# Kernel optimization log

Measured on AMD Instinct MI355X. Metric: run time of the kernel, lower is better.

Reference implementation:

```python
import jax, jax.numpy as jnp
import numpy as np

DIM = 2048
N_HEADS = 16
N_KV_HEADS = 4
HEAD_DIM = DIM // N_HEADS  # 128
T = 2048


def setup_inputs() -> dict:
    key = jax.random.key(0)
    k1, k2, k3 = jax.random.split(key, 3)
    scale = 1.0 / np.sqrt(DIM)
    x = jax.random.normal(k1, (T, DIM), dtype=jnp.float32)
    # GQA-consistent fused QKV projection: q (n_h*hd) + k (n_kv*hd) + v (n_kv*hd)
    qkv_out = (N_HEADS + 2 * N_KV_HEADS) * HEAD_DIM  # 3072
    W_qkv = jax.random.normal(k2, (DIM, qkv_out), dtype=jnp.float32) * scale
    W_o = jax.random.normal(k3, (N_HEADS * HEAD_DIM, DIM), dtype=jnp.float32) * scale
    return {"x": x, "W_qkv": W_qkv, "W_o": W_o}


def reference(x, W_qkv, W_o):
    Tn, C = x.shape
    hd = HEAD_DIM
    qkv = x @ W_qkv  # [T, (n_h + 2*n_kv)*hd]
    q, k, v = jnp.split(qkv, [N_HEADS * hd, (N_HEADS + N_KV_HEADS) * hd], axis=-1)
    q = q.reshape(Tn, N_HEADS, hd).transpose(1, 0, 2)      # [n_h, T, hd]
    k = k.reshape(Tn, N_KV_HEADS, hd).transpose(1, 0, 2)   # [n_kv, T, hd]
    v = v.reshape(Tn, N_KV_HEADS, hd).transpose(1, 0, 2)
    rep = N_HEADS // N_KV_HEADS
    k = jnp.repeat(k, rep, axis=0)  # [n_h, T, hd]
    v = jnp.repeat(v, rep, axis=0)
    scores = jnp.einsum('hid,hjd->hij', q, k) / jnp.sqrt(jnp.asarray(hd, x.dtype))
    causal = jnp.tril(jnp.ones((Tn, Tn), dtype=bool))[None, :, :]
    scores = jnp.where(causal, scores, -jnp.inf)
    attn = jax.nn.softmax(scores, axis=-1)
    out = jnp.einsum('hij,hjd->hid', attn, v)  # [n_h, T, hd]
    out = out.transpose(1, 0, 2).reshape(Tn, N_HEADS * hd)
    return out @ W_o
```

## Files before the change

kernel.cpp:

```cpp
#include <hip/hip_runtime.h>
#include <stdint.h>

#define T_SEQ   2048
#define DMODEL  2048
#define NH      16
#define HD      128
#define QKVN    3072
#define KCOL    2048
#define VCOL    2560

typedef __bf16 bf16x8 __attribute__((ext_vector_type(8)));
typedef float  f32x4  __attribute__((ext_vector_type(4)));
typedef unsigned short u16x8 __attribute__((ext_vector_type(8)));

__device__ __forceinline__ uint16_t f2bf(float f) {
    uint32_t u = __builtin_bit_cast(uint32_t, f);
    u += 0x7fffu + ((u >> 16) & 1u);
    return (uint16_t)(u >> 16);
}
__device__ __forceinline__ float bf2f(uint16_t u) {
    return __builtin_bit_cast(float, (uint32_t)u << 16);
}
__device__ __forceinline__ u16x8 ld8(const uint16_t* p) {
    return *reinterpret_cast<const u16x8*>(p);
}
__device__ __forceinline__ void st8(uint16_t* p, u16x8 v) {
    *reinterpret_cast<u16x8*>(p) = v;
}
__device__ __forceinline__ bf16x8 as_bf(u16x8 v) { return __builtin_bit_cast(bf16x8, v); }

__device__ __forceinline__ uint32_t cvtpk(float a, float b) {
    uint32_t r;
    asm("v_cvt_pk_bf16_f32 %0, %1, %2" : "=v"(r) : "v"(a), "v"(b));
    return r;
}

__device__ __forceinline__ void gl_lds16(const uint16_t* g, uint16_t* l) {
    __builtin_amdgcn_global_load_lds((const __attribute__((address_space(1))) void*)g,
                                     (__attribute__((address_space(3))) void*)l, 16, 0, 0);
}

__global__ __launch_bounds__(256) void k_cast(const float* __restrict__ in,
                                              uint16_t* __restrict__ out, int n8) {
    int i = blockIdx.x * 256 + threadIdx.x;
    if (i >= n8) return;
    const f32x4* p = reinterpret_cast<const f32x4*>(in) + (size_t)i * 2;
    f32x4 a = p[0], b = p[1];
    u16x8 o;
    o[0] = f2bf(a[0]); o[1] = f2bf(a[1]); o[2] = f2bf(a[2]); o[3] = f2bf(a[3]);
    o[4] = f2bf(b[0]); o[5] = f2bf(b[1]); o[6] = f2bf(b[2]); o[7] = f2bf(b[3]);
    reinterpret_cast<u16x8*>(out)[i] = o;
}

__global__ __launch_bounds__(256) void k_tcast(const float* __restrict__ in,
                                               uint16_t* __restrict__ out, int R, int C) {
    __shared__ uint16_t tile[64][72];
    int t = threadIdx.x;
    int rbase = blockIdx.y * 64, cbase = blockIdx.x * 64;
#pragma unroll
    for (int p = 0; p < 4; ++p) {
        int ir = p * 16 + (t >> 4);
        int ic = (t & 15) * 4;
        f32x4 v = *reinterpret_cast<const f32x4*>(&in[(size_t)(rbase + ir) * C + cbase + ic]);
        tile[ir][ic + 0] = f2bf(v[0]);
        tile[ir][ic + 1] = f2bf(v[1]);
        tile[ir][ic + 2] = f2bf(v[2]);
        tile[ir][ic + 3] = f2bf(v[3]);
    }
    __syncthreads();
#pragma unroll
    for (int p = 0; p < 2; ++p) {
        int oc = p * 32 + (t >> 3);
        int orr = (t & 7) * 8;
        u16x8 o;
#pragma unroll
        for (int e = 0; e < 8; ++e) o[e] = tile[orr + e][oc];
        st8(&out[(size_t)(cbase + oc) * R + rbase + orr], o);
    }
}

__global__ __launch_bounds__(256) void k_tbf16(const uint16_t* __restrict__ in,
                                               uint16_t* __restrict__ out,
                                               int R, int C, int ldin, int coff) {
    __shared__ uint16_t tile[64][72];
    int t = threadIdx.x;
    int rbase = blockIdx.y * 64, cbase = blockIdx.x * 64;
#pragma unroll
    for (int p = 0; p < 2; ++p) {
        int ir = p * 32 + (t >> 3);
        int ic = (t & 7) * 8;
        u16x8 v = ld8(&in[(size_t)(rbase + ir) * ldin + coff + cbase + ic]);
#pragma unroll
        for (int e = 0; e < 8; ++e) tile[ir][ic + e] = v[e];
    }
    __syncthreads();
#pragma unroll
    for (int p = 0; p < 2; ++p) {
        int oc = p * 32 + (t >> 3);
        int orr = (t & 7) * 8;
        u16x8 o;
#pragma unroll
        for (int e = 0; e < 8; ++e) o[e] = tile[orr + e][oc];
        st8(&out[(size_t)(cbase + oc) * R + rbase + orr], o);
    }
}

__global__ __launch_bounds__(256) void k_gemm(const uint16_t* __restrict__ A,
                                              const uint16_t* __restrict__ Bt,
                                              void* __restrict__ Cout,
                                              int M, int N, int K, int gy,
                                              int out_bf16, int scale_cols, float qscale) {
    __shared__ __align__(16) uint16_t Asm[2][64 * 64];
    __shared__ __align__(16) uint16_t Bsm[2][128 * 64];
    int t = threadIdx.x;
    int w = t >> 6, lane = t & 63, lo = lane & 15, g4 = lane >> 4;

    int nwg = (int)gridDim.x;
    int wg = (int)blockIdx.x;
    int idx = (wg & 7) * (nwg >> 3) + (wg >> 3);
    int bx = idx / gy, by = idx % gy;
    int mbase = by * 64, nbase = bx * 128;

    int wm = w >> 1, wn = w & 1;

    const uint16_t* pA[2]; int lofsA[2];
#pragma unroll
    for (int c = 0; c < 2; ++c) {
        int ch = w * 2 + c;
        int r = ch * 8 + (lane >> 3);
        pA[c] = A + (size_t)(mbase + r) * K + (((lane & 7) ^ (r & 7)) * 8);
        lofsA[c] = ch * 512;
    }
    const uint16_t* pB[4]; int lofsB[4];
#pragma unroll
    for (int c = 0; c < 4; ++c) {
        int ch = w * 4 + c;
        int r = ch * 8 + (lane >> 3);
        pB[c] = Bt + (size_t)(nbase + r) * K + (((lane & 7) ^ (r & 7)) * 8);
        lofsB[c] = ch * 512;
    }

    f32x4 acc[2][4] = {};

#pragma unroll
    for (int c = 0; c < 2; ++c) gl_lds16(pA[c], &Asm[0][lofsA[c]]);
#pragma unroll
    for (int c = 0; c < 4; ++c) gl_lds16(pB[c], &Bsm[0][lofsB[c]]);

    int cur = 0;
    for (int kt = 0; kt < K; kt += 64) {
        __syncthreads();
        if (kt + 64 < K) {
            int ko = kt + 64;
#pragma unroll
            for (int c = 0; c < 2; ++c) gl_lds16(pA[c] + ko, &Asm[cur ^ 1][lofsA[c]]);
#pragma unroll
            for (int c = 0; c < 4; ++c) gl_lds16(pB[c] + ko, &Bsm[cur ^ 1][lofsB[c]]);
        }
        bf16x8 af[2][2], bfr[2][4];
#pragma unroll
        for (int ks = 0; ks < 2; ++ks) {
#pragma unroll
            for (int i = 0; i < 2; ++i) {
                int ar = wm * 32 + i * 16 + lo;
                af[ks][i] = as_bf(ld8(&Asm[cur][(ar * 64 + ks * 32 + g4 * 8) ^ ((lo & 7) << 3)]));
            }
#pragma unroll
            for (int j = 0; j < 4; ++j) {
                int br = wn * 64 + j * 16 + lo;
                bfr[ks][j] = as_bf(ld8(&Bsm[cur][(br * 64 + ks * 32 + g4 * 8) ^ ((lo & 7) << 3)]));
            }
        }
        __builtin_amdgcn_s_setprio(1);
#pragma unroll
        for (int ks = 0; ks < 2; ++ks)
#pragma unroll
            for (int i = 0; i < 2; ++i)
#pragma unroll
                for (int j = 0; j < 4; ++j)
                    acc[i][j] = __builtin_amdgcn_mfma_f32_16x16x32_bf16(af[ks][i], bfr[ks][j], acc[i][j], 0, 0, 0);
        __builtin_amdgcn_s_setprio(0);
        cur ^= 1;
    }

    if (out_bf16) {
        uint16_t* C = (uint16_t*)Cout;
#pragma unroll
        for (int i = 0; i < 2; ++i)
#pragma unroll
            for (int j = 0; j < 4; ++j)
#pragma unroll
                for (int r = 0; r < 4; ++r) {
                    int row = mbase + wm * 32 + i * 16 + g4 * 4 + r;
                    int col = nbase + wn * 64 + j * 16 + lo;
                    float v = acc[i][j][r];
                    if (col < scale_cols) v *= qscale;
                    C[(size_t)row * N + col] = f2bf(v);
                }
    } else {
        float* C = (float*)Cout;
#pragma unroll
        for (int i = 0; i < 2; ++i)
#pragma unroll
            for (int j = 0; j < 4; ++j)
#pragma unroll
                for (int r = 0; r < 4; ++r) {
                    int row = mbase + wm * 32 + i * 16 + g4 * 4 + r;
                    int col = nbase + wn * 64 + j * 16 + lo;
                    C[(size_t)row * N + col] = acc[i][j][r];
                }
    }
}

__global__ __launch_bounds__(256) void k_attn(const uint16_t* __restrict__ qkv,
                                              const uint16_t* __restrict__ vt,
                                              uint16_t* __restrict__ po,
                                              float* __restrict__ pml) {
    __shared__ __align__(16) uint16_t Ksm[2][32 * 128];
    __shared__ __align__(16) uint16_t Vsm[2][128 * 32];
    __shared__ __align__(16) uint16_t Psm[4][16 * 40];
    int t = threadIdx.x;
    int w = t >> 6, lane = t & 63, lo = lane & 15, g4 = lane >> 4;
    int x = blockIdx.x, h = blockIdx.y, sp = blockIdx.z, kh = h >> 2;

    const uint16_t* kbase = qkv + KCOL + (size_t)kh * HD;
    const uint16_t* vbase = vt + (size_t)(kh * HD) * T_SEQ;

    const uint16_t* kp[2]; const uint16_t* vp[2]; int lofs[2];
#pragma unroll
    for (int c = 0; c < 2; ++c) {
        int ch = w * 2 + c;
        int kr = ch * 4 + (lane >> 4);
        kp[c] = kbase + (size_t)kr * QKVN + ((lane & 15) ^ (kr & 7)) * 8;
        int vr = ch * 16 + (lane >> 2);
        vp[c] = vbase + (size_t)vr * T_SEQ + (lane & 3) * 8;
        lofs[c] = ch * 512;
    }

    for (int rep = 0; rep < 2; ++rep) {
        int qt = rep ? 31 - x : x;
        int qb = qt * 64;
        int cnt = (2 * qt + 4 - sp) / 3;

        bf16x8 qf[4];
        {
            int qrow = qb + w * 16 + lo;
            const uint16_t* qp = &qkv[(size_t)qrow * QKVN + h * HD + g4 * 8];
#pragma unroll
            for (int ks = 0; ks < 4; ++ks) qf[ks] = as_bf(ld8(qp + ks * 32));
        }

        f32x4 o[8] = {};
        float mr = -INFINITY, pp = 0.f;

        if (cnt) {
            __syncthreads();
            size_t ko = (size_t)sp * 32 * QKVN; int vo = sp * 32;
#pragma unroll
            for (int c = 0; c < 2; ++c) {
                gl_lds16(kp[c] + ko, &Ksm[0][lofs[c]]);
                gl_lds16(vp[c] + vo, &Vsm[0][lofs[c]]);
            }
        }

        int cur = 0;
        for (int it = 0; it < cnt; ++it) {
            int jt = sp + 3 * it;
            __syncthreads();
            if (it + 1 < cnt) {
                size_t ko = (size_t)(jt + 3) * 32 * QKVN;
                int vo = (jt + 3) * 32;
#pragma unroll
                for (int c = 0; c < 2; ++c) {
                    gl_lds16(kp[c] + ko, &Ksm[cur ^ 1][lofs[c]]);
                    gl_lds16(vp[c] + vo, &Vsm[cur ^ 1][lofs[c]]);
                }
            }

            f32x4 s[2] = {};
            __builtin_amdgcn_s_setprio(1);
#pragma unroll
            for (int nt = 0; nt < 2; ++nt) {
                int j = nt * 16 + lo;
#pragma unroll
                for (int ks = 0; ks < 4; ++ks) {
                    bf16x8 a = as_bf(ld8(&Ksm[cur][(j * 128 + ks * 32 + g4 * 8) ^ ((lo & 7) << 3)]));
                    s[nt] = __builtin_amdgcn_mfma_f32_16x16x32_bf16(a, qf[ks], s[nt], 0, 0, 0);
                }
            }
            __builtin_amdgcn_s_setprio(0);

            if (jt >= 2 * qt) {
                int jb = jt * 32;
                int i = qb + w * 16 + lo;
#pragma unroll
                for (int nt = 0; nt < 2; ++nt)
#pragma unroll
                    for (int r = 0; r < 4; ++r) {
                        int j = jb + nt * 16 + g4 * 4 + r;
                        if (j > i) s[nt][r] = -INFINITY;
                    }
            }

            float pm = fmaxf(fmaxf(fmaxf(s[0][0], s[0][1]), fmaxf(s[0][2], s[0][3])),
                             fmaxf(fmaxf(s[1][0], s[1][1]), fmaxf(s[1][2], s[1][3])));
            pm = fmaxf(pm, __shfl_xor(pm, 16));
            pm = fmaxf(pm, __shfl_xor(pm, 32));

            if (__any(pm > mr + 11.f)) {
                float mn = fmaxf(mr, pm);
                float msafe_old = fmaxf(mr, -1e30f);
                float al = exp2f(fminf(msafe_old - mn, 0.f));
                mr = mn;
                pp *= al;
                float alo[4];
#pragma unroll
                for (int r = 0; r < 4; ++r)
                    alo[r] = __shfl(al, (lane & 48) | (((lane >> 4) << 2) + r));
#pragma unroll
                for (int dt = 0; dt < 8; ++dt)
#pragma unroll
                    for (int r = 0; r < 4; ++r) o[dt][r] *= alo[r];
            }
            float msafe = fmaxf(mr, -1e30f);
#pragma unroll
            for (int nt = 0; nt < 2; ++nt)
#pragma unroll
                for (int r = 0; r < 4; ++r) {
                    float pe = exp2f(s[nt][r] - msafe);
                    s[nt][r] = pe;
                    pp += pe;
                }
#pragma unroll
            for (int nt = 0; nt < 2; ++nt) {
                uint32_t p01 = cvtpk(s[nt][0], s[nt][1]);
                uint32_t p23 = cvtpk(s[nt][2], s[nt][3]);
                *reinterpret_cast<uint2*>(&Psm[w][lo * 40 + nt * 16 + g4 * 4]) =
                    make_uint2(p01, p23);
            }

            bf16x8 pa = as_bf(ld8(&Psm[w][lo * 40 + g4 * 8]));
            __builtin_amdgcn_s_setprio(1);
#pragma unroll
            for (int dt = 0; dt < 8; ++dt) {
                int d = dt * 16 + lo;
                bf16x8 vb = as_bf(ld8(&Vsm[cur][d * 32 + g4 * 8]));
                o[dt] = __builtin_amdgcn_mfma_f32_16x16x32_bf16(pa, vb, o[dt], 0, 0, 0);
            }
            __builtin_amdgcn_s_setprio(0);
            cur ^= 1;
        }

        float lr = pp;
        lr += __shfl_xor(lr, 16);
        lr += __shfl_xor(lr, 32);

        uint16_t* pob = po + (size_t)sp * T_SEQ * DMODEL;
#pragma unroll
        for (int dt = 0; dt < 8; ++dt)
#pragma unroll
            for (int r = 0; r < 4; ++r) {
                int i = qb + w * 16 + g4 * 4 + r;
                int col = h * HD + dt * 16 + lo;
                pob[(size_t)i * DMODEL + col] = f2bf(o[dt][r]);
            }
        if (lane < 16) {
            int i = qb + w * 16 + lane;
            float* pe = pml + (size_t)sp * T_SEQ * NH * 2 + ((size_t)i * NH + h) * 2;
            pe[0] = mr;
            pe[1] = lr;
        }
    }
}

__global__ __launch_bounds__(256) void k_comb(uint16_t* __restrict__ po,
                                              const float* __restrict__ pml) {
    int i = blockIdx.x * 256 + threadIdx.x;
    int row = i >> 8;
    int cg = i & 255;
    int h = cg >> 4;
    int col = cg * 8;
    const size_t PS = (size_t)T_SEQ * NH * 2;
    const size_t TD = (size_t)T_SEQ * DMODEL;
    size_t mo = ((size_t)row * NH + h) * 2;
    float m0 = pml[mo], l0 = pml[mo + 1];
    float m1 = pml[PS + mo], l1 = pml[PS + mo + 1];
    float m2 = pml[2 * PS + mo], l2 = pml[2 * PS + mo + 1];
    float m = fmaxf(fmaxf(m0, m1), m2);
    float w0 = exp2f(m0 - m), w1 = exp2f(m1 - m), w2 = exp2f(m2 - m);
    float rl = 1.f / (l0 * w0 + l1 * w1 + l2 * w2);
    size_t off = (size_t)row * DMODEL + col;
    u16x8 a = ld8(po + off);
    u16x8 b = ld8(po + TD + off);
    u16x8 c = ld8(po + 2 * TD + off);
    u16x8 o;
#pragma unroll
    for (int e = 0; e < 8; ++e)
        o[e] = f2bf((bf2f(a[e]) * w0 + bf2f(b[e]) * w1 + bf2f(c[e]) * w2) * rl);
    st8(po + off, o);
}

extern "C" void kernel_launch(void* const* d_in, const int* in_sizes, int n_in,
                              void* d_out, int out_size, void* d_ws, size_t ws_size,
                              hipStream_t stream) {
    (void)in_sizes; (void)n_in; (void)out_size; (void)ws_size;
    const float* x    = (const float*)d_in[0];
    const float* Wqkv = (const float*)d_in[1];
    const float* Wo   = (const float*)d_in[2];
    float* out = (float*)d_out;

    char* ws = (char*)d_ws;
    uint16_t* xb   = (uint16_t*)(ws + 0);
    uint16_t* wqt  = (uint16_t*)(ws + 8388608);
    uint16_t* po   = (uint16_t*)(ws + 0);
    float*    pml  = (float*)(ws + 25165824);
    uint16_t* wot  = (uint16_t*)(ws + 25952256);
    uint16_t* qkvb = (uint16_t*)(ws + 34340864);
    uint16_t* vtb  = (uint16_t*)(ws + 46923776);

    const float qscale = 0.12751743f;

    k_cast<<<2048, 256, 0, stream>>>(x, xb, 524288);
    k_tcast<<<dim3(48, 32), 256, 0, stream>>>(Wqkv, wqt, 2048, 3072);
    k_tcast<<<dim3(32, 32), 256, 0, stream>>>(Wo, wot, 2048, 2048);
    k_gemm<<<768, 256, 0, stream>>>(xb, wqt, qkvb, 2048, 3072, 2048, 32, 1, 2048, qscale);
    k_tbf16<<<dim3(8, 32), 256, 0, stream>>>(qkvb, vtb, 2048, 512, 3072, 2560);
    k_attn<<<dim3(16, 16, 3), 256, 0, stream>>>(qkvb, vtb, po, pml);
    k_comb<<<2048, 256, 0, stream>>>(po, pml);
    k_gemm<<<512, 256, 0, stream>>>(po, wot, out, 2048, 2048, 2048, 32, 0, 0, 1.0f);
}
```

Measured before the change: 155.8 us.

## Use 64-wide KV tiles and a 2-way KV split in attention

The attention kernel now processes 64-key tiles instead of 32, doubling the K/V shared-memory buffers and the P staging width. The KV sequence is split two ways across the grid instead of three, and the combine kernel merges two partials. V tiles in LDS are XOR-swizzled to avoid bank conflicts. The aim is fewer barriers and online-softmax rescale steps per key, and less partial-output traffic. In exchange there are fewer blocks (512 vs 768), higher LDS use per block and more wasted work on diagonal tiles.

After: 133.7 us. 14.2% less time.

```diff
diff --git a/kernel.cpp b/kernel.cpp
--- a/kernel.cpp
+++ b/kernel.cpp
@@ -216,31 +216,31 @@
                                               const uint16_t* __restrict__ vt,
                                               uint16_t* __restrict__ po,
                                               float* __restrict__ pml) {
-    __shared__ __align__(16) uint16_t Ksm[2][32 * 128];
-    __shared__ __align__(16) uint16_t Vsm[2][128 * 32];
-    __shared__ __align__(16) uint16_t Psm[4][16 * 40];
+    __shared__ __align__(16) uint16_t Ksm[2][64 * 128];
+    __shared__ __align__(16) uint16_t Vsm[2][128 * 64];
+    __shared__ __align__(16) uint16_t Psm[4][16 * 72];
     int t = threadIdx.x;
     int w = t >> 6, lane = t & 63, lo = lane & 15, g4 = lane >> 4;
-    int x = blockIdx.x, h = blockIdx.y, sp = blockIdx.z, kh = h >> 2;
+    int x = blockIdx.x, h = blockIdx.y, p = blockIdx.z, kh = h >> 2;
 
     const uint16_t* kbase = qkv + KCOL + (size_t)kh * HD;
     const uint16_t* vbase = vt + (size_t)(kh * HD) * T_SEQ;
 
-    const uint16_t* kp[2]; const uint16_t* vp[2]; int lofs[2];
-#pragma unroll
-    for (int c = 0; c < 2; ++c) {
-        int ch = w * 2 + c;
+    const uint16_t* kp[4]; const uint16_t* vp[4]; int lofs[4];
+#pragma unroll
+    for (int c = 0; c < 4; ++c) {
+        int ch = w * 4 + c;
         int kr = ch * 4 + (lane >> 4);
         kp[c] = kbase + (size_t)kr * QKVN + ((lane & 15) ^ (kr & 7)) * 8;
-        int vr = ch * 16 + (lane >> 2);
-        vp[c] = vbase + (size_t)vr * T_SEQ + (lane & 3) * 8;
+        int vr = ch * 8 + (lane >> 3);
+        vp[c] = vbase + (size_t)vr * T_SEQ + ((lane & 7) ^ (vr & 7)) * 8;
         lofs[c] = ch * 512;
     }
 
     for (int rep = 0; rep < 2; ++rep) {
         int qt = rep ? 31 - x : x;
         int qb = qt * 64;
-        int cnt = (2 * qt + 4 - sp) / 3;
+        int cnt = (qt + 2 - p) >> 1;
 
         bf16x8 qf[4];
         {
@@ -255,9 +255,9 @@
 
         if (cnt) {
             __syncthreads();
-            size_t ko = (size_t)sp * 32 * QKVN; int vo = sp * 32;
-#pragma unroll
-            for (int c = 0; c < 2; ++c) {
+            size_t ko = (size_t)p * 64 * QKVN; int vo = p * 64;
+#pragma unroll
+            for (int c = 0; c < 4; ++c) {
                 gl_lds16(kp[c] + ko, &Ksm[0][lofs[c]]);
                 gl_lds16(vp[c] + vo, &Vsm[0][lofs[c]]);
             }
@@ -265,22 +265,22 @@
 
         int cur = 0;
         for (int it = 0; it < cnt; ++it) {
-            int jt = sp + 3 * it;
+            int jt = p + 2 * it;
             __syncthreads();
             if (it + 1 < cnt) {
-                size_t ko = (size_t)(jt + 3) * 32 * QKVN;
-                int vo = (jt + 3) * 32;
-#pragma unroll
-                for (int c = 0; c < 2; ++c) {
+                size_t ko = (size_t)(jt + 2) * 64 * QKVN;
+                int vo = (jt + 2) * 64;
+#pragma unroll
+                for (int c = 0; c < 4; ++c) {
                     gl_lds16(kp[c] + ko, &Ksm[cur ^ 1][lofs[c]]);
                     gl_lds16(vp[c] + vo, &Vsm[cur ^ 1][lofs[c]]);
                 }
             }
 
-            f32x4 s[2] = {};
+            f32x4 s[4] = {};
             __builtin_amdgcn_s_setprio(1);
 #pragma unroll
-            for (int nt = 0; nt < 2; ++nt) {
+            for (int nt = 0; nt < 4; ++nt) {
                 int j = nt * 16 + lo;
 #pragma unroll
                 for (int ks = 0; ks < 4; ++ks) {
@@ -290,11 +290,11 @@
             }
             __builtin_amdgcn_s_setprio(0);
 
-            if (jt >= 2 * qt) {
-                int jb = jt * 32;
+            if (jt == qt) {
                 int i = qb + w * 16 + lo;
-#pragma unroll
-                for (int nt = 0; nt < 2; ++nt)
+                int jb = jt * 64;
+#pragma unroll
+                for (int nt = 0; nt < 4; ++nt)
 #pragma unroll
                     for (int r = 0; r < 4; ++r) {
                         int j = jb + nt * 16 + g4 * 4 + r;
@@ -302,15 +302,17 @@
                     }
             }
 
-            float pm = fmaxf(fmaxf(fmaxf(s[0][0], s[0][1]), fmaxf(s[0][2], s[0][3])),
-                             fmaxf(fmaxf(s[1][0], s[1][1]), fmaxf(s[1][2], s[1][3])));
+            float pm = fmaxf(
+                fmaxf(fmaxf(fmaxf(s[0][0], s[0][1]), fmaxf(s[0][2], s[0][3])),
+                      fmaxf(fmaxf(s[1][0], s[1][1]), fmaxf(s[1][2], s[1][3]))),
+                fmaxf(fmaxf(fmaxf(s[2][0], s[2][1]), fmaxf(s[2][2], s[2][3])),
+                      fmaxf(fmaxf(s[3][0], s[3][1]), fmaxf(s[3][2], s[3][3]))));
             pm = fmaxf(pm, __shfl_xor(pm, 16));
             pm = fmaxf(pm, __shfl_xor(pm, 32));
 
             if (__any(pm > mr + 11.f)) {
                 float mn = fmaxf(mr, pm);
-                float msafe_old = fmaxf(mr, -1e30f);
-                float al = exp2f(fminf(msafe_old - mn, 0.f));
+                float al = exp2f(fminf(fmaxf(mr, -1e30f) - mn, 0.f));
                 mr = mn;
                 pp *= al;
                 float alo[4];
@@ -324,7 +326,7 @@
             }
             float msafe = fmaxf(mr, -1e30f);
 #pragma unroll
-            for (int nt = 0; nt < 2; ++nt)
+            for (int nt = 0; nt < 4; ++nt)
 #pragma unroll
                 for (int r = 0; r < 4; ++r) {
                     float pe = exp2f(s[nt][r] - msafe);
@@ -332,20 +334,23 @@
                     pp += pe;
                 }
 #pragma unroll
-            for (int nt = 0; nt < 2; ++nt) {
+            for (int nt = 0; nt < 4; ++nt) {
                 uint32_t p01 = cvtpk(s[nt][0], s[nt][1]);
                 uint32_t p23 = cvtpk(s[nt][2], s[nt][3]);
-                *reinterpret_cast<uint2*>(&Psm[w][lo * 40 + nt * 16 + g4 * 4]) =
+                *reinterpret_cast<uint2*>(&Psm[w][lo * 72 + nt * 16 + g4 * 4]) =
                     make_uint2(p01, p23);
             }
 
-            bf16x8 pa = as_bf(ld8(&Psm[w][lo * 40 + g4 * 8]));
             __builtin_amdgcn_s_setprio(1);
 #pragma unroll
-            for (int dt = 0; dt < 8; ++dt) {
-                int d = dt * 16 + lo;
-                bf16x8 vb = as_bf(ld8(&Vsm[cur][d * 32 + g4 * 8]));
-                o[dt] = __builtin_amdgcn_mfma_f32_16x16x32_bf16(pa, vb, o[dt], 0, 0, 0);
+            for (int ks2 = 0; ks2 < 2; ++ks2) {
+                bf16x8 pa = as_bf(ld8(&Psm[w][lo * 72 + ks2 * 32 + g4 * 8]));
+#pragma unroll
+                for (int dt = 0; dt < 8; ++dt) {
+                    int d = dt * 16 + lo;
+                    bf16x8 vb = as_bf(ld8(&Vsm[cur][(d * 64 + ks2 * 32 + g4 * 8) ^ ((lo & 7) << 3)]));
+                    o[dt] = __builtin_amdgcn_mfma_f32_16x16x32_bf16(pa, vb, o[dt], 0, 0, 0);
+                }
             }
             __builtin_amdgcn_s_setprio(0);
             cur ^= 1;
@@ -355,7 +360,7 @@
         lr += __shfl_xor(lr, 16);
         lr += __shfl_xor(lr, 32);
 
-        uint16_t* pob = po + (size_t)sp * T_SEQ * DMODEL;
+        uint16_t* pob = po + (size_t)p * T_SEQ * DMODEL;
 #pragma unroll
         for (int dt = 0; dt < 8; ++dt)
 #pragma unroll
@@ -366,7 +371,7 @@
             }
         if (lane < 16) {
             int i = qb + w * 16 + lane;
-            float* pe = pml + (size_t)sp * T_SEQ * NH * 2 + ((size_t)i * NH + h) * 2;
+            float* pe = pml + (size_t)p * T_SEQ * NH * 2 + ((size_t)i * NH + h) * 2;
             pe[0] = mr;
             pe[1] = lr;
         }
@@ -385,18 +390,16 @@
     size_t mo = ((size_t)row * NH + h) * 2;
     float m0 = pml[mo], l0 = pml[mo + 1];
     float m1 = pml[PS + mo], l1 = pml[PS + mo + 1];
-    float m2 = pml[2 * PS + mo], l2 = pml[2 * PS + mo + 1];
-    float m = fmaxf(fmaxf(m0, m1), m2);
-    float w0 = exp2f(m0 - m), w1 = exp2f(m1 - m), w2 = exp2f(m2 - m);
-    float rl = 1.f / (l0 * w0 + l1 * w1 + l2 * w2);
+    float m = fmaxf(m0, m1);
+    float w0 = exp2f(m0 - m), w1 = exp2f(m1 - m);
+    float rl = 1.f / (l0 * w0 + l1 * w1);
     size_t off = (size_t)row * DMODEL + col;
     u16x8 a = ld8(po + off);
     u16x8 b = ld8(po + TD + off);
-    u16x8 c = ld8(po + 2 * TD + off);
     u16x8 o;
 #pragma unroll
     for (int e = 0; e < 8; ++e)
-        o[e] = f2bf((bf2f(a[e]) * w0 + bf2f(b[e]) * w1 + bf2f(c[e]) * w2) * rl);
+        o[e] = f2bf((bf2f(a[e]) * w0 + bf2f(b[e]) * w1) * rl);
     st8(po + off, o);
 }
 
@@ -413,10 +416,10 @@
     uint16_t* xb   = (uint16_t*)(ws + 0);
     uint16_t* wqt  = (uint16_t*)(ws + 8388608);
     uint16_t* po   = (uint16_t*)(ws + 0);
-    float*    pml  = (float*)(ws + 25165824);
-    uint16_t* wot  = (uint16_t*)(ws + 25952256);
-    uint16_t* qkvb = (uint16_t*)(ws + 34340864);
-    uint16_t* vtb  = (uint16_t*)(ws + 46923776);
+    float*    pml  = (float*)(ws + 16777216);
+    uint16_t* wot  = (uint16_t*)(ws + 20971520);
+    uint16_t* qkvb = (uint16_t*)(ws + 29360128);
+    uint16_t* vtb  = (uint16_t*)(ws + 41943040);
 
     const float qscale = 0.12751743f;
 
@@ -425,7 +428,7 @@
     k_tcast<<<dim3(32, 32), 256, 0, stream>>>(Wo, wot, 2048, 2048);
     k_gemm<<<768, 256, 0, stream>>>(xb, wqt, qkvb, 2048, 3072, 2048, 32, 1, 2048, qscale);
     k_tbf16<<<dim3(8, 32), 256, 0, stream>>>(qkvb, vtb, 2048, 512, 3072, 2560);
-    k_attn<<<dim3(16, 16, 3), 256, 0, stream>>>(qkvb, vtb, po, pml);
+    k_attn<<<dim3(16, 16, 2), 256, 0, stream>>>(qkvb, vtb, po, pml);
     k_comb<<<2048, 256, 0, stream>>>(po, pml);
     k_gemm<<<512, 256, 0, stream>>>(po, wot, out, 2048, 2048, 2048, 32, 0, 0, 1.0f);
 }
```
